# Optimization experiments

Measured on AMD Instinct MI355X. Metric: run time of the kernel, lower is better.

The kernel has to match this reference:

```python
import jax, jax.numpy as jnp
import numpy as np

B = 131072
NE, NR, D = 500000, 1000, 128
MARGIN = 1.0
EPS = 1e-6  # torch PairwiseDistance default eps


def setup_inputs() -> dict:
    key = jax.random.key(0)
    ks = jax.random.split(key, 10)
    def triples(k1, k2, k3):
        h = jax.random.randint(k1, (B, 1), 0, NE)
        r = jax.random.randint(k2, (B, 1), 0, NR)
        t = jax.random.randint(k3, (B, 1), 0, NE)
        return jnp.concatenate([h, r, t], axis=1)  # (B, 3)
    posX = triples(ks[0], ks[1], ks[2])
    negX = triples(ks[3], ks[4], ks[5])
    W_e = jax.random.normal(ks[6], (NE, D), dtype=jnp.float32)
    W_ep = jax.random.normal(ks[7], (NE, D), dtype=jnp.float32)
    W_r = jax.random.normal(ks[8], (NR, D), dtype=jnp.float32)
    W_rp = jax.random.normal(ks[9], (NR, D), dtype=jnp.float32)
    return {"posX": posX, "negX": negX, "W_e": W_e, "W_ep": W_ep,
            "W_r": W_r, "W_rp": W_rp}


def _score(X, W_e, W_ep, W_r, W_rp):
    # X: (B, 3) int triples [head, relation, tail]
    h, r, t = X[:, 0], X[:, 1], X[:, 2]
    head, headp = W_e[h], W_ep[h]        # (B, D)
    tail, tailp = W_e[t], W_ep[t]        # (B, D)
    rel, relp = W_r[r], W_rp[r]          # (B, D)
    # Mrh = relp ⊗ headp + I (Em == En), so Mrh @ head = head + relp * (headp·head)
    hm = head + relp * jnp.sum(headp * head, axis=-1, keepdims=True)
    tm = tail + relp * jnp.sum(tailp * tail, axis=-1, keepdims=True)
    diff = hm + rel - tm + EPS
    return jnp.sqrt(jnp.sum(diff * diff, axis=-1))  # L2 pairwise distance


def reference(posX, negX, W_e, W_ep, W_r, W_rp):
    pos = _score(posX, W_e, W_ep, W_r, W_rp)
    neg = _score(negX, W_e, W_ep, W_r, W_rp)
    return jnp.sum(jax.nn.relu(pos - neg + MARGIN)) / posX.shape[0]
```

## Files before the change

kernel.cpp:

```cpp
#include <hip/hip_runtime.h>

#define D 128
#define MARGIN 1.0f
#define EPS 1e-6f
#define NB 2048
#define WPB 4

__global__ __launch_bounds__(256, 8) void transd_main(
    const int* __restrict__ posX, const int* __restrict__ negX,
    const float* __restrict__ W_e, const float* __restrict__ W_ep,
    const float* __restrict__ W_r, const float* __restrict__ W_rp,
    float* __restrict__ out, int nTriples)
{
    const int tid  = threadIdx.x;
    const int wid  = tid >> 6;
    const int lane = tid & 63;
    const int l4   = (lane & 31) * 4;
    const int* __restrict__ X = (lane >= 32) ? negX : posX;

    const int gw = blockIdx.x * WPB + wid;
    const int nw = NB * WPB;

    float acc = 0.0f;

    for (int b = gw; b < nTriples; b += nw) {
        const int h = X[b * 3 + 0];
        const int r = X[b * 3 + 1];
        const int t = X[b * 3 + 2];

        const size_t ho = (size_t)h * D + l4;
        const size_t to = (size_t)t * D + l4;
        const size_t ro = (size_t)r * D + l4;

        const float4 head  = *(const float4*)(W_e  + ho);
        const float4 headp = *(const float4*)(W_ep + ho);
        const float4 tail  = *(const float4*)(W_e  + to);
        const float4 tailp = *(const float4*)(W_ep + to);
        const float4 rel   = *(const float4*)(W_r  + ro);
        const float4 relp  = *(const float4*)(W_rp + ro);

        float dh = headp.x * head.x + headp.y * head.y + headp.z * head.z + headp.w * head.w;
        float dt = tailp.x * tail.x + tailp.y * tail.y + tailp.z * tail.z + tailp.w * tail.w;

        #pragma unroll
        for (int m = 1; m <= 16; m <<= 1) {
            dh += __shfl_xor(dh, m, 64);
            dt += __shfl_xor(dt, m, 64);
        }
        const float dd = dh - dt;

        float4 diff;
        diff.x = fmaf(relp.x, dd, head.x - tail.x + rel.x + EPS);
        diff.y = fmaf(relp.y, dd, head.y - tail.y + rel.y + EPS);
        diff.z = fmaf(relp.z, dd, head.z - tail.z + rel.z + EPS);
        diff.w = fmaf(relp.w, dd, head.w - tail.w + rel.w + EPS);

        float ss = diff.x * diff.x + diff.y * diff.y + diff.z * diff.z + diff.w * diff.w;
        #pragma unroll
        for (int m = 1; m <= 16; m <<= 1) ss += __shfl_xor(ss, m, 64);

        const float score = sqrtf(ss);
        const float other = __shfl_xor(score, 32, 64);

        if (lane == 0) acc += fmaxf(0.0f, score - other + MARGIN);
    }

    __shared__ float sacc[WPB];
    if (lane == 0) sacc[wid] = acc;
    __syncthreads();
    if (tid == 0) {
        float s = 0.0f;
        #pragma unroll
        for (int i = 0; i < WPB; ++i) s += sacc[i];
        atomicAdd(out, s / (float)nTriples);
    }
}

extern "C" void kernel_launch(void* const* d_in, const int* in_sizes, int n_in,
                              void* d_out, int out_size, void* d_ws, size_t ws_size,
                              hipStream_t stream) {
    const int*   posX = (const int*)d_in[0];
    const int*   negX = (const int*)d_in[1];
    const float* W_e  = (const float*)d_in[2];
    const float* W_ep = (const float*)d_in[3];
    const float* W_r  = (const float*)d_in[4];
    const float* W_rp = (const float*)d_in[5];
    float* out = (float*)d_out;

    const int nTriples = in_sizes[0] / 3;

    hipMemsetAsync(out, 0, sizeof(float), stream);
    hipLaunchKernelGGL(transd_main, dim3(NB), dim3(256), 0, stream,
                       posX, negX, W_e, W_ep, W_r, W_rp, out, nTriples);
}
```

Measured before the change: 97.73 us.

## Prefetch next triple indices, merge dot reductions, replace atomics with reduce kernel

Each wave now loads the next iteration's (h,r,t) indices while it processes the current one, so the dependent index-load then gather chain is partly overlapped. The two dot-product shuffle reductions are merged into one reduction of their difference. The per-block atomicAdd and the memset are replaced by per-block partials in workspace plus a second single-block reduce kernel. This adds a second launch, and the merged reduction changes the floating-point summation order slightly.

Measured after the change: 95.58 us. 1.02x faster.

```diff
diff --git a/kernel.cpp b/kernel.cpp
--- a/kernel.cpp
+++ b/kernel.cpp
@@ -10,7 +10,7 @@
     const int* __restrict__ posX, const int* __restrict__ negX,
     const float* __restrict__ W_e, const float* __restrict__ W_ep,
     const float* __restrict__ W_r, const float* __restrict__ W_rp,
-    float* __restrict__ out, int nTriples)
+    float* __restrict__ partials, int nTriples)
 {
     const int tid  = threadIdx.x;
     const int wid  = tid >> 6;
@@ -21,16 +21,25 @@
     const int gw = blockIdx.x * WPB + wid;
     const int nw = NB * WPB;
 
+    const int iters = (gw < nTriples) ? ((nTriples - 1 - gw) / nw + 1) : 0;
+
     float acc = 0.0f;
 
-    for (int b = gw; b < nTriples; b += nw) {
-        const int h = X[b * 3 + 0];
-        const int r = X[b * 3 + 1];
-        const int t = X[b * 3 + 2];
+    int h = 0, r = 0, t = 0;
+    if (iters > 0) {
+        h = X[gw * 3 + 0]; r = X[gw * 3 + 1]; t = X[gw * 3 + 2];
+    }
 
+    for (int i = 0; i < iters; ++i) {
         const size_t ho = (size_t)h * D + l4;
         const size_t to = (size_t)t * D + l4;
         const size_t ro = (size_t)r * D + l4;
+
+        int nh = h, nr = r, nt = t;
+        if (i + 1 < iters) {
+            const int nb = gw + (i + 1) * nw;
+            nh = X[nb * 3 + 0]; nr = X[nb * 3 + 1]; nt = X[nb * 3 + 2];
+        }
 
         const float4 head  = *(const float4*)(W_e  + ho);
         const float4 headp = *(const float4*)(W_ep + ho);
@@ -39,15 +48,13 @@
         const float4 rel   = *(const float4*)(W_r  + ro);
         const float4 relp  = *(const float4*)(W_rp + ro);
 
-        float dh = headp.x * head.x + headp.y * head.y + headp.z * head.z + headp.w * head.w;
-        float dt = tailp.x * tail.x + tailp.y * tail.y + tailp.z * tail.z + tailp.w * tail.w;
-
+        float dpart = headp.x * head.x + headp.y * head.y
+                    + headp.z * head.z + headp.w * head.w
+                    - tailp.x * tail.x - tailp.y * tail.y
+                    - tailp.z * tail.z - tailp.w * tail.w;
         #pragma unroll
-        for (int m = 1; m <= 16; m <<= 1) {
-            dh += __shfl_xor(dh, m, 64);
-            dt += __shfl_xor(dt, m, 64);
-        }
-        const float dd = dh - dt;
+        for (int m = 1; m <= 16; m <<= 1) dpart += __shfl_xor(dpart, m, 64);
+        const float dd = dpart;
 
         float4 diff;
         diff.x = fmaf(relp.x, dd, head.x - tail.x + rel.x + EPS);
@@ -63,6 +70,8 @@
         const float other = __shfl_xor(score, 32, 64);
 
         if (lane == 0) acc += fmaxf(0.0f, score - other + MARGIN);
+
+        h = nh; r = nr; t = nt;
     }
 
     __shared__ float sacc[WPB];
@@ -72,8 +81,23 @@
         float s = 0.0f;
         #pragma unroll
         for (int i = 0; i < WPB; ++i) s += sacc[i];
-        atomicAdd(out, s / (float)nTriples);
+        partials[blockIdx.x] = s;
     }
+}
+
+__global__ void transd_reduce(const float* __restrict__ partial, int n,
+                              float* __restrict__ out, int nTriples)
+{
+    __shared__ float s[256];
+    float v = 0.0f;
+    for (int i = threadIdx.x; i < n; i += 256) v += partial[i];
+    s[threadIdx.x] = v;
+    __syncthreads();
+    for (int k = 128; k > 0; k >>= 1) {
+        if ((int)threadIdx.x < k) s[threadIdx.x] += s[threadIdx.x + k];
+        __syncthreads();
+    }
+    if (threadIdx.x == 0) out[0] = s[0] / (float)nTriples;
 }
 
 extern "C" void kernel_launch(void* const* d_in, const int* in_sizes, int n_in,
@@ -89,7 +113,9 @@
 
     const int nTriples = in_sizes[0] / 3;
 
-    hipMemsetAsync(out, 0, sizeof(float), stream);
+    float* partials = (float*)d_ws;
     hipLaunchKernelGGL(transd_main, dim3(NB), dim3(256), 0, stream,
-                       posX, negX, W_e, W_ep, W_r, W_rp, out, nTriples);
+                       posX, negX, W_e, W_ep, W_r, W_rp, partials, nTriples);
+    hipLaunchKernelGGL(transd_reduce, dim3(1), dim3(256), 0, stream,
+                       partials, NB, out, nTriples);
 }
```
